# Kernel tuning notes

Measured on AMD Instinct MI355X. Metric: run time of the kernel, lower is better.

Reference implementation:

```python
import jax, jax.numpy as jnp
import numpy as np

IN_DIM = 512
OUT_DIM = 512


def setup_inputs() -> dict:
    key = jax.random.key(0)
    ks = jax.random.split(key, 7)
    B, S = 4, 2048
    scale = 1.0 / np.sqrt(IN_DIM)
    X = jax.random.normal(ks[0], (B, S, IN_DIM), dtype=jnp.float32)
    Wq = jax.random.normal(ks[1], (IN_DIM, OUT_DIM), dtype=jnp.float32) * scale
    Wk = jax.random.normal(ks[2], (IN_DIM, OUT_DIM), dtype=jnp.float32) * scale
    Wv = jax.random.normal(ks[3], (IN_DIM, OUT_DIM), dtype=jnp.float32) * scale
    bq = jnp.zeros((OUT_DIM,), dtype=jnp.float32)
    bk = jnp.zeros((OUT_DIM,), dtype=jnp.float32)
    bv = jnp.zeros((OUT_DIM,), dtype=jnp.float32)
    return {"X": X, "Wq": Wq, "bq": bq, "Wk": Wk, "bk": bk, "Wv": Wv, "bv": bv}


def reference(X, Wq, bq, Wk, bk, Wv, bv):
    # Q/K/V projections: [B,S,in] @ [in,out] -> [B,S,out]
    Q = X @ Wq + bq
    K = X @ Wk + bk
    V = X @ Wv + bv
    d_k = jnp.asarray(Q.shape[-1], Q.dtype)
    # scores: [B,S,S] = QK^T / sqrt(d_k)
    scores = jnp.einsum('bsd,btd->bst', Q, K) / jnp.sqrt(d_k)
    attn = jax.nn.softmax(scores, axis=-1)
    # out: [B,S,out]
    return jnp.einsum('bst,btd->bsd', attn, V)
```

## Files before the change

### kernel.cpp

```cpp
#include <hip/hip_runtime.h>
#include <hip/hip_bf16.h>
#include <stdint.h>

#define SEQ   2048
#define DIM   512
#define BATCH 4

typedef __attribute__((ext_vector_type(8))) short  short8;
typedef __attribute__((ext_vector_type(4))) float  floatx4;

static __device__ __forceinline__ unsigned short f2b(float f) {
  return __builtin_bit_cast(unsigned short, __float2bfloat16(f));
}

static __device__ __forceinline__ void gll16(const void* g, void* l) {
  __builtin_amdgcn_global_load_lds(
      (__attribute__((address_space(1))) void*)(uintptr_t)g,
      (__attribute__((address_space(3))) void*)l, 16, 0, 0);
}


template <int AF, int BF, int WM, int WN, int KC, int PH, int KIT, int NW>
__device__ __forceinline__ void fgemm_p(
    const char* __restrict__ A, int rtA0, int TKA,
    const char* __restrict__ B, int rtB0, int TKB,
    char* lds, floatx4 (&acc)[AF / WM][BF / WN])
{
  constexpr int AWF  = AF / WM, BWF = BF / WN;
  constexpr int SLOT = (AF + BF) * KC * 1024;
  constexpr int L    = KC * (AF / NW + BF / NW);
  constexpr int AC   = AWF / PH;
  static_assert(KIT >= 3, "pipeline needs >=3 K-slots");
  static_assert(AF % NW == 0 && BF % NW == 0, "frag rows must divide waves");
  static_assert(AWF % PH == 0 && L % PH == 0, "phase split must divide");
  const int tid = threadIdx.x;
  const int w = tid >> 6, l = tid & 63;
  const int wm = w % WM, wn = w / WM;

  auto stage_part = [&](char* dst, int kt, int p) {
#pragma unroll
    for (int g = p * (L / PH); g < (p + 1) * (L / PH); ++g) {
      if (g < KC * (AF / NW)) {
        const int c = g / (AF / NW), q = g % (AF / NW);
        const int f = q * NW + w;
        gll16(A + (((size_t)(rtA0 + f) * TKA + kt * KC + c) << 10) + l * 16,
              dst + (c * AF + f) * 1024 + l * 16);
      } else {
        const int h = g - KC * (AF / NW);
        const int c = h / (BF / NW), q = h % (BF / NW);
        const int f = q * NW + w;
        gll16(B + (((size_t)(rtB0 + f) * TKB + kt * KC + c) << 10) + l * 16,
              dst + (KC * AF + c * BF + f) * 1024 + l * 16);
      }
    }
  };

#pragma unroll
  for (int p = 0; p < PH; ++p) stage_part(lds, 0, p);
#pragma unroll
  for (int p = 0; p < PH; ++p) stage_part(lds + SLOT, 1, p);
  asm volatile("s_waitcnt vmcnt(%0) lgkmcnt(0)\ns_barrier" :: "n"(L) : "memory");

  short8 bf[KC][BWF];
  int cs = 0;
#pragma unroll 2
  for (int kt = 0; kt < KIT; ++kt) {
    const char* bA = lds + cs * SLOT;
    const char* bB = bA + KC * AF * 1024;
    int ns = cs - 1; if (ns < 0) ns = 2;
    char* pdst = lds + ns * SLOT;
#pragma unroll
    for (int p = 0; p < PH; ++p) {
      short8 af[KC][AC];
#pragma unroll
      for (int c = 0; c < KC; ++c)
#pragma unroll
        for (int i = 0; i < AC; ++i)
          af[c][i] = *(const short8*)(bA + (c * AF + wm * AWF + p * AC + i) * 1024 + l * 16);
      if (p == 0) {
#pragma unroll
        for (int c = 0; c < KC; ++c)
#pragma unroll
          for (int j = 0; j < BWF; ++j)
            bf[c][j] = *(const short8*)(bB + (c * BF + wn * BWF + j) * 1024 + l * 16);
      }
      if (kt + 2 < KIT) stage_part(pdst, kt + 2, p);

      asm volatile("s_barrier" ::: "memory");
      asm volatile("s_waitcnt lgkmcnt(0)" ::: "memory");
      __builtin_amdgcn_s_setprio(1);
#pragma unroll
      for (int c = 0; c < KC; ++c)
#pragma unroll
        for (int i = 0; i < AC; ++i)
#pragma unroll
          for (int j = 0; j < BWF; ++j)
            acc[p * AC + i][j] = __builtin_amdgcn_mfma_f32_16x16x32_bf16(
                af[c][i], bf[c][j], acc[p * AC + i][j], 0, 0, 0);
      __builtin_amdgcn_s_setprio(0);

      if (p == PH - 1) {
        if (kt + 2 < KIT)
          asm volatile("s_waitcnt vmcnt(%0)\ns_barrier" :: "n"(L) : "memory");
        else if (kt + 1 < KIT)
          asm volatile("s_waitcnt vmcnt(0)\ns_barrier" ::: "memory");
      } else {
        asm volatile("s_barrier" ::: "memory");
      }
    }
    ++cs; if (cs == 3) cs = 0;
  }
}

__global__ __launch_bounds__(256) void setup_kernel(
    const float* __restrict__ X, const float* __restrict__ Wq,
    const float* __restrict__ Wk, const float* __restrict__ Wv,
    short8* __restrict__ XbF, short8* __restrict__ WF)
{
  const int flat = blockIdx.x * 256 + threadIdx.x;
  {
    const int tile = flat >> 6, l = flat & 63;
    const int row = (tile >> 4) * 16 + (l & 15);
    const int k0  = (tile & 15) * 32 + (l >> 4) * 8;
    const float4 v0 = *(const float4*)(X + (size_t)row * DIM + k0);
    const float4 v1 = *(const float4*)(X + (size_t)row * DIM + k0 + 4);
    short8 o;
    o[0] = (short)f2b(v0.x); o[1] = (short)f2b(v0.y);
    o[2] = (short)f2b(v0.z); o[3] = (short)f2b(v0.w);
    o[4] = (short)f2b(v1.x); o[5] = (short)f2b(v1.y);
    o[6] = (short)f2b(v1.z); o[7] = (short)f2b(v1.w);
    XbF[flat] = o;
  }
  if (flat < 3 * 32768) {
    const int z = flat >> 15, within = flat & 32767;
    const float* W = (z == 0) ? Wq : (z == 1) ? Wk : Wv;
    const int tile = within >> 6, l = within & 63;
    const int n  = (tile >> 4) * 16 + (l & 15);
    const int k0 = (tile & 15) * 32 + (l >> 4) * 8;
    short8 o;
#pragma unroll
    for (int e = 0; e < 8; ++e)
      o[e] = (short)f2b(W[(size_t)(k0 + e) * DIM + n]);
    WF[flat] = o;
  }
}

__global__ __launch_bounds__(256, 2) void qkv_kernel(
    const short8* __restrict__ XbF, const short8* __restrict__ WF,
    const float* __restrict__ bq, const float* __restrict__ bk,
    const float* __restrict__ bv,
    unsigned short* __restrict__ QF, unsigned short* __restrict__ KF,
    unsigned short* __restrict__ VF)
{
  __shared__ char lds[73728];
  const int blk = blockIdx.x;
  const int n = (blk & 7) * 48 + (blk >> 3);
  const int lane = threadIdx.x & 63, w = threadIdx.x >> 6;
  const int wm = w & 1, wn = w >> 1;
  const char* Xc = (const char*)XbF;
  const char* Wc = (const char*)WF;
  floatx4 acc[8][4] = {};

  if (n < 256) {
    const int z = n >> 7, y = (n >> 6) & 1, x = n & 63;
    fgemm_p<16, 8, 2, 2, 1, 2, 16, 4>(Wc + (size_t)z * 524288, y * 16, 16,
                                      Xc, x * 8, 16, lds, acc);
    const float* bias = z ? bk : bq;
    unsigned short* OF = z ? KF : QF;
    const int dbase = y * 256 + wm * 128;
    const int sbase = x * 128 + wn * 64;
#pragma unroll
    for (int i2 = 0; i2 < 8; ++i2) {
      const int d0 = dbase + i2 * 16 + (lane >> 4) * 4;
      const float4 b4 = *(const float4*)(bias + d0);
#pragma unroll
      for (int j = 0; j < 4; ++j) {
        const int s = sbase + j * 16 + (lane & 15);
        ushort4 pk;
        pk.x = f2b(acc[i2][j][0] + b4.x);
        pk.y = f2b(acc[i2][j][1] + b4.y);
        pk.z = f2b(acc[i2][j][2] + b4.z);
        pk.w = f2b(acc[i2][j][3] + b4.w);
        *(ushort4*)(OF + (size_t)((s >> 4) * 16 + (d0 >> 5)) * 512 +
                    ((((d0 & 31) >> 3) << 4) | (s & 15)) * 8 + (d0 & 7)) = pk;
      }
    }
  } else {
    const int m = n - 256;
    const int x = m >> 2, y = m & 3;
    fgemm_p<16, 8, 2, 2, 1, 2, 16, 4>(Xc, x * 16, 16,
                                      Wc + 2 * 524288, y * 8, 16, lds, acc);
    const int sbase = x * 256 + wm * 128;
    const int dbase = y * 128 + wn * 64;
#pragma unroll
    for (int i2 = 0; i2 < 8; ++i2) {
      const int s0 = sbase + i2 * 16 + (lane >> 4) * 4;
      const int bt = s0 >> 11, t0 = s0 & 2047;
#pragma unroll
      for (int j = 0; j < 4; ++j) {
        const int d = dbase + j * 16 + (lane & 15);
        const float bn = bv[d];
        ushort4 pk;
        pk.x = f2b(acc[i2][j][0] + bn);
        pk.y = f2b(acc[i2][j][1] + bn);
        pk.z = f2b(acc[i2][j][2] + bn);
        pk.w = f2b(acc[i2][j][3] + bn);
        *(ushort4*)(VF + (size_t)bt * DIM * SEQ +
                    (size_t)((d >> 4) * 64 + (t0 >> 5)) * 512 +
                    ((((t0 & 31) >> 3) << 4) | (d & 15)) * 8 + (t0 & 7)) = pk;
      }
    }
  }
}

__global__ __launch_bounds__(512, 2) void scores_kernel(
    const unsigned short* __restrict__ QF, const unsigned short* __restrict__ KF,
    unsigned short* __restrict__ ScF, float* __restrict__ prow)
{
  __shared__ char lds[98304];
  const int blk = blockIdx.x;
  const int n = (blk & 7) * 32 + (blk >> 3);
  const int b = n >> 6, y = (n >> 3) & 7, x = n & 7;
  const int lane = threadIdx.x & 63, w = threadIdx.x >> 6;
  const int wm = w & 1, wn = w >> 1;
  floatx4 acc[8][4] = {};
  fgemm_p<16, 16, 2, 4, 1, 2, 16, 8>((const char*)KF + (size_t)b * 2097152, y * 16, 16,
                                     (const char*)QF + (size_t)b * 2097152, x * 16, 16,
                                     lds, acc);

  unsigned short* S = ScF + (size_t)b * SEQ * SEQ;
  const float scale = 0.044194173824159216f;
  const int tbase = y * 256 + wm * 128;
  const int sbase = x * 256 + wn * 64;
  float colsum[4] = {0.f, 0.f, 0.f, 0.f};
#pragma unroll
  for (int i2 = 0; i2 < 8; ++i2) {
    const int t0 = tbase + i2 * 16 + (lane >> 4) * 4;
#pragma unroll
    for (int j = 0; j < 4; ++j) {
      const int s = sbase + j * 16 + (lane & 15);
      float e0 = __expf(acc[i2][j][0] * scale);
      float e1 = __expf(acc[i2][j][1] * scale);
      float e2 = __expf(acc[i2][j][2] * scale);
      float e3 = __expf(acc[i2][j][3] * scale);
      colsum[j] += (e0 + e1) + (e2 + e3);
      ushort4 pk;
      pk.x = f2b(e0); pk.y = f2b(e1); pk.z = f2b(e2); pk.w = f2b(e3);
      *(ushort4*)(S + (size_t)((s >> 4) * 64 + (t0 >> 5)) * 512 +
                  ((((t0 & 31) >> 3) << 4) | (s & 15)) * 8 + (t0 & 7)) = pk;
    }
  }
#pragma unroll
  for (int j = 0; j < 4; ++j) {
    colsum[j] += __shfl_xor(colsum[j], 16, 64);
    colsum[j] += __shfl_xor(colsum[j], 32, 64);
  }
  if (lane < 16) {
    float* dst = prow + ((size_t)(y * 2 + wm) * BATCH + b) * SEQ + sbase + lane;
#pragma unroll
    for (int j = 0; j < 4; ++j) dst[j * 16] = colsum[j];
  }
}

__global__ __launch_bounds__(512, 2) void pv_kernel(
    const unsigned short* __restrict__ ScF, const unsigned short* __restrict__ VF,
    const float* __restrict__ prow, float* __restrict__ out)
{
  __shared__ char lds[98304];
  __shared__ float rinv[128];
  const int blk = blockIdx.x;
  const int n = (blk & 7) * 32 + (blk >> 3);
  const int b = n >> 6, x = (n >> 2) & 15, y = n & 3;
  const int t = threadIdx.x;
  if (t < 128) {
    const int s = x * 128 + t;
    float rr = 0.f;
#pragma unroll
    for (int q = 0; q < 16; ++q) rr += prow[((size_t)q * BATCH + b) * SEQ + s];
    rinv[t] = 1.f / rr;
  }
  const int lane = threadIdx.x & 63, w = threadIdx.x >> 6;
  const int wm = w & 1, wn = w >> 1;
  floatx4 acc[4][2] = {};
  fgemm_p<8, 8, 2, 4, 2, 1, 32, 8>((const char*)ScF + (size_t)b * 8388608, x * 8, 64,
                                   (const char*)VF + (size_t)b * 2097152, y * 8, 64,
                                   lds, acc);

  const int mbase = x * 128 + wm * 64;
  const int dbase = y * 128 + wn * 32;
#pragma unroll
  for (int i2 = 0; i2 < 4; ++i2) {
    const int r0 = wm * 64 + i2 * 16 + (lane >> 4) * 4;
    const int m0 = mbase + i2 * 16 + (lane >> 4) * 4;
    const float inv0 = rinv[r0], inv1 = rinv[r0 + 1], inv2 = rinv[r0 + 2], inv3 = rinv[r0 + 3];
#pragma unroll
    for (int j = 0; j < 2; ++j) {
      const int d = dbase + j * 16 + (lane & 15);
      float* o = out + ((size_t)b * SEQ + m0) * DIM + d;
      o[0 * DIM] = acc[i2][j][0] * inv0;
      o[1 * DIM] = acc[i2][j][1] * inv1;
      o[2 * DIM] = acc[i2][j][2] * inv2;
      o[3 * DIM] = acc[i2][j][3] * inv3;
    }
  }
}

extern "C" void kernel_launch(void* const* d_in, const int* in_sizes, int n_in,
                              void* d_out, int out_size, void* d_ws, size_t ws_size,
                              hipStream_t stream) {
  const float* X  = (const float*)d_in[0];
  const float* Wq = (const float*)d_in[1];
  const float* bq = (const float*)d_in[2];
  const float* Wk = (const float*)d_in[3];
  const float* bk = (const float*)d_in[4];
  const float* Wv = (const float*)d_in[5];
  const float* bv = (const float*)d_in[6];
  float* out = (float*)d_out;
  char* ws = (char*)d_ws;

  short8* XbF = (short8*)(ws + 0);
  float*  prow = (float*)(ws + 0);
  short8* WF  = (short8*)(ws + 8388608);
  unsigned short* QF  = (unsigned short*)(ws + 9961472);
  unsigned short* KF  = (unsigned short*)(ws + 18350080);
  unsigned short* VF  = (unsigned short*)(ws + 26738688);
  unsigned short* ScF = (unsigned short*)(ws + 35127296);

  setup_kernel<<<dim3(2048), 256, 0, stream>>>(X, Wq, Wk, Wv, XbF, WF);
  qkv_kernel<<<dim3(384), 256, 0, stream>>>(XbF, WF, bq, bk, bv, QF, KF, VF);
  scores_kernel<<<dim3(256), 512, 0, stream>>>(QF, KF, ScF, prow);
  pv_kernel<<<dim3(256), 512, 0, stream>>>(ScF, VF, prow, out);
}
```

Before: 140.7 us.

## Replace LDS-staged GEMM pipeline with direct global-to-register fragment loads

Drops the triple-buffered global_load_lds staging and its barriers. Each wave now loads its MFMA fragments straight from global memory into registers, using optional register double-buffering in the PV GEMM. The retiling gives qkv 8 waves per block and the scores kernel 512 blocks with narrower tiles, so the prow partial count goes from 16 to 32. Fragments shared across waves are no longer reused through LDS, which means more redundant global/L2 traffic and more exposed load latency in exchange for having no synchronisation.

After: 155.2 us. 10.4% more time.

```diff
diff --git a/kernel.cpp b/kernel.cpp
--- a/kernel.cpp
+++ b/kernel.cpp
@@ -13,102 +13,55 @@
   return __builtin_bit_cast(unsigned short, __float2bfloat16(f));
 }
 
-static __device__ __forceinline__ void gll16(const void* g, void* l) {
-  __builtin_amdgcn_global_load_lds(
-      (__attribute__((address_space(1))) void*)(uintptr_t)g,
-      (__attribute__((address_space(3))) void*)l, 16, 0, 0);
-}
-
-
-template <int AF, int BF, int WM, int WN, int KC, int PH, int KIT, int NW>
-__device__ __forceinline__ void fgemm_p(
+template <int AF, int BF, int WM, int WN, int KIT, bool DB>
+__device__ __forceinline__ void fgemm_d(
     const char* __restrict__ A, int rtA0, int TKA,
     const char* __restrict__ B, int rtB0, int TKB,
-    char* lds, floatx4 (&acc)[AF / WM][BF / WN])
-{
-  constexpr int AWF  = AF / WM, BWF = BF / WN;
-  constexpr int SLOT = (AF + BF) * KC * 1024;
-  constexpr int L    = KC * (AF / NW + BF / NW);
-  constexpr int AC   = AWF / PH;
-  static_assert(KIT >= 3, "pipeline needs >=3 K-slots");
-  static_assert(AF % NW == 0 && BF % NW == 0, "frag rows must divide waves");
-  static_assert(AWF % PH == 0 && L % PH == 0, "phase split must divide");
+    floatx4 (&acc)[AF / WM][BF / WN])
+{
+  constexpr int AWF = AF / WM, BWF = BF / WN;
   const int tid = threadIdx.x;
   const int w = tid >> 6, l = tid & 63;
   const int wm = w % WM, wn = w / WM;
-
-  auto stage_part = [&](char* dst, int kt, int p) {
-#pragma unroll
-    for (int g = p * (L / PH); g < (p + 1) * (L / PH); ++g) {
-      if (g < KC * (AF / NW)) {
-        const int c = g / (AF / NW), q = g % (AF / NW);
-        const int f = q * NW + w;
-        gll16(A + (((size_t)(rtA0 + f) * TKA + kt * KC + c) << 10) + l * 16,
-              dst + (c * AF + f) * 1024 + l * 16);
-      } else {
-        const int h = g - KC * (AF / NW);
-        const int c = h / (BF / NW), q = h % (BF / NW);
-        const int f = q * NW + w;
-        gll16(B + (((size_t)(rtB0 + f) * TKB + kt * KC + c) << 10) + l * 16,
-              dst + (KC * AF + c * BF + f) * 1024 + l * 16);
-      }
-    }
+  const char* Ab = A + (((size_t)(rtA0 + wm * AWF) * TKA) << 10) + l * 16;
+  const char* Bb = B + (((size_t)(rtB0 + wn * BWF) * TKB) << 10) + l * 16;
+
+  auto lda = [&](short8 (&af)[AWF], int kt) {
+#pragma unroll
+    for (int i = 0; i < AWF; ++i)
+      af[i] = *(const short8*)(Ab + (((size_t)i * TKA + kt) << 10));
   };
-
-#pragma unroll
-  for (int p = 0; p < PH; ++p) stage_part(lds, 0, p);
-#pragma unroll
-  for (int p = 0; p < PH; ++p) stage_part(lds + SLOT, 1, p);
-  asm volatile("s_waitcnt vmcnt(%0) lgkmcnt(0)\ns_barrier" :: "n"(L) : "memory");
-
-  short8 bf[KC][BWF];
-  int cs = 0;
+  auto ldb = [&](short8 (&bf)[BWF], int kt) {
+#pragma unroll
+    for (int j = 0; j < BWF; ++j)
+      bf[j] = *(const short8*)(Bb + (((size_t)j * TKB + kt) << 10));
+  };
+  auto domfma = [&](short8 (&af)[AWF], short8 (&bf)[BWF]) {
+#pragma unroll
+    for (int i = 0; i < AWF; ++i)
+#pragma unroll
+      for (int j = 0; j < BWF; ++j)
+        acc[i][j] = __builtin_amdgcn_mfma_f32_16x16x32_bf16(af[i], bf[j], acc[i][j], 0, 0, 0);
+  };
+
+  if constexpr (DB) {
+    short8 a0[AWF], b0[BWF], a1[AWF], b1[BWF];
+    lda(a0, 0); ldb(b0, 0);
+    static_assert(KIT % 2 == 0, "DB path needs even KIT");
 #pragma unroll 2
-  for (int kt = 0; kt < KIT; ++kt) {
-    const char* bA = lds + cs * SLOT;
-    const char* bB = bA + KC * AF * 1024;
-    int ns = cs - 1; if (ns < 0) ns = 2;
-    char* pdst = lds + ns * SLOT;
-#pragma unroll
-    for (int p = 0; p < PH; ++p) {
-      short8 af[KC][AC];
-#pragma unroll
-      for (int c = 0; c < KC; ++c)
-#pragma unroll
-        for (int i = 0; i < AC; ++i)
-          af[c][i] = *(const short8*)(bA + (c * AF + wm * AWF + p * AC + i) * 1024 + l * 16);
-      if (p == 0) {
-#pragma unroll
-        for (int c = 0; c < KC; ++c)
-#pragma unroll
-          for (int j = 0; j < BWF; ++j)
-            bf[c][j] = *(const short8*)(bB + (c * BF + wn * BWF + j) * 1024 + l * 16);
-      }
-      if (kt + 2 < KIT) stage_part(pdst, kt + 2, p);
-
-      asm volatile("s_barrier" ::: "memory");
-      asm volatile("s_waitcnt lgkmcnt(0)" ::: "memory");
-      __builtin_amdgcn_s_setprio(1);
-#pragma unroll
-      for (int c = 0; c < KC; ++c)
-#pragma unroll
-        for (int i = 0; i < AC; ++i)
-#pragma unroll
-          for (int j = 0; j < BWF; ++j)
-            acc[p * AC + i][j] = __builtin_amdgcn_mfma_f32_16x16x32_bf16(
-                af[c][i], bf[c][j], acc[p * AC + i][j], 0, 0, 0);
-      __builtin_amdgcn_s_setprio(0);
-
-      if (p == PH - 1) {
-        if (kt + 2 < KIT)
-          asm volatile("s_waitcnt vmcnt(%0)\ns_barrier" :: "n"(L) : "memory");
-        else if (kt + 1 < KIT)
-          asm volatile("s_waitcnt vmcnt(0)\ns_barrier" ::: "memory");
-      } else {
-        asm volatile("s_barrier" ::: "memory");
-      }
-    }
-    ++cs; if (cs == 3) cs = 0;
+    for (int kt = 0; kt < KIT; kt += 2) {
+      lda(a1, kt + 1); ldb(b1, kt + 1);
+      domfma(a0, b0);
+      if (kt + 2 < KIT) { lda(a0, kt + 2); ldb(b0, kt + 2); }
+      domfma(a1, b1);
+    }
+  } else {
+#pragma unroll 2
+    for (int kt = 0; kt < KIT; ++kt) {
+      short8 af[AWF], bf[BWF];
+      lda(af, kt); ldb(bf, kt);
+      domfma(af, bf);
+    }
   }
 }
 
@@ -145,32 +98,31 @@
   }
 }
 
-__global__ __launch_bounds__(256, 2) void qkv_kernel(
+__global__ __launch_bounds__(512, 2) void qkv_kernel(
     const short8* __restrict__ XbF, const short8* __restrict__ WF,
     const float* __restrict__ bq, const float* __restrict__ bk,
     const float* __restrict__ bv,
     unsigned short* __restrict__ QF, unsigned short* __restrict__ KF,
     unsigned short* __restrict__ VF)
 {
-  __shared__ char lds[73728];
   const int blk = blockIdx.x;
   const int n = (blk & 7) * 48 + (blk >> 3);
   const int lane = threadIdx.x & 63, w = threadIdx.x >> 6;
-  const int wm = w & 1, wn = w >> 1;
+  const int wm = w & 3, wn = w >> 2;
   const char* Xc = (const char*)XbF;
   const char* Wc = (const char*)WF;
-  floatx4 acc[8][4] = {};
+  floatx4 acc[4][4] = {};
 
   if (n < 256) {
     const int z = n >> 7, y = (n >> 6) & 1, x = n & 63;
-    fgemm_p<16, 8, 2, 2, 1, 2, 16, 4>(Wc + (size_t)z * 524288, y * 16, 16,
-                                      Xc, x * 8, 16, lds, acc);
+    fgemm_d<16, 8, 4, 2, 16, false>(Wc + (size_t)z * 524288, y * 16, 16,
+                                    Xc, x * 8, 16, acc);
     const float* bias = z ? bk : bq;
     unsigned short* OF = z ? KF : QF;
-    const int dbase = y * 256 + wm * 128;
+    const int dbase = y * 256 + wm * 64;
     const int sbase = x * 128 + wn * 64;
 #pragma unroll
-    for (int i2 = 0; i2 < 8; ++i2) {
+    for (int i2 = 0; i2 < 4; ++i2) {
       const int d0 = dbase + i2 * 16 + (lane >> 4) * 4;
       const float4 b4 = *(const float4*)(bias + d0);
 #pragma unroll
@@ -188,12 +140,12 @@
   } else {
     const int m = n - 256;
     const int x = m >> 2, y = m & 3;
-    fgemm_p<16, 8, 2, 2, 1, 2, 16, 4>(Xc, x * 16, 16,
-                                      Wc + 2 * 524288, y * 8, 16, lds, acc);
-    const int sbase = x * 256 + wm * 128;
+    fgemm_d<16, 8, 4, 2, 16, false>(Xc, x * 16, 16,
+                                    Wc + 2 * 524288, y * 8, 16, acc);
+    const int sbase = x * 256 + wm * 64;
     const int dbase = y * 128 + wn * 64;
 #pragma unroll
-    for (int i2 = 0; i2 < 8; ++i2) {
+    for (int i2 = 0; i2 < 4; ++i2) {
       const int s0 = sbase + i2 * 16 + (lane >> 4) * 4;
       const int bt = s0 >> 11, t0 = s0 & 2047;
 #pragma unroll
@@ -217,24 +169,24 @@
     const unsigned short* __restrict__ QF, const unsigned short* __restrict__ KF,
     unsigned short* __restrict__ ScF, float* __restrict__ prow)
 {
-  __shared__ char lds[98304];
   const int blk = blockIdx.x;
-  const int n = (blk & 7) * 32 + (blk >> 3);
-  const int b = n >> 6, y = (n >> 3) & 7, x = n & 7;
+  const int n = (blk & 7) * 64 + (blk >> 3);
+  const int b = n >> 7, t = n & 127;
+  const int y = t >> 4, x = t & 15;
   const int lane = threadIdx.x & 63, w = threadIdx.x >> 6;
-  const int wm = w & 1, wn = w >> 1;
-  floatx4 acc[8][4] = {};
-  fgemm_p<16, 16, 2, 4, 1, 2, 16, 8>((const char*)KF + (size_t)b * 2097152, y * 16, 16,
-                                     (const char*)QF + (size_t)b * 2097152, x * 16, 16,
-                                     lds, acc);
+  const int wm = w & 3, wn = w >> 2;
+  floatx4 acc[4][4] = {};
+  fgemm_d<16, 8, 4, 2, 16, false>((const char*)KF + (size_t)b * 2097152, y * 16, 16,
+                                  (const char*)QF + (size_t)b * 2097152, x * 8, 16,
+                                  acc);
 
   unsigned short* S = ScF + (size_t)b * SEQ * SEQ;
   const float scale = 0.044194173824159216f;
-  const int tbase = y * 256 + wm * 128;
-  const int sbase = x * 256 + wn * 64;
+  const int tbase = y * 256 + wm * 64;
+  const int sbase = x * 128 + wn * 64;
   float colsum[4] = {0.f, 0.f, 0.f, 0.f};
 #pragma unroll
-  for (int i2 = 0; i2 < 8; ++i2) {
+  for (int i2 = 0; i2 < 4; ++i2) {
     const int t0 = tbase + i2 * 16 + (lane >> 4) * 4;
 #pragma unroll
     for (int j = 0; j < 4; ++j) {
@@ -256,7 +208,7 @@
     colsum[j] += __shfl_xor(colsum[j], 32, 64);
   }
   if (lane < 16) {
-    float* dst = prow + ((size_t)(y * 2 + wm) * BATCH + b) * SEQ + sbase + lane;
+    float* dst = prow + ((size_t)(y * 4 + wm) * BATCH + b) * SEQ + sbase + lane;
 #pragma unroll
     for (int j = 0; j < 4; ++j) dst[j * 16] = colsum[j];
   }
@@ -266,35 +218,36 @@
     const unsigned short* __restrict__ ScF, const unsigned short* __restrict__ VF,
     const float* __restrict__ prow, float* __restrict__ out)
 {
-  __shared__ char lds[98304];
   __shared__ float rinv[128];
   const int blk = blockIdx.x;
   const int n = (blk & 7) * 32 + (blk >> 3);
-  const int b = n >> 6, x = (n >> 2) & 15, y = n & 3;
+  const int b = n >> 6, r = n & 63;
+  const int x = r >> 2, y = r & 3;
   const int t = threadIdx.x;
   if (t < 128) {
     const int s = x * 128 + t;
     float rr = 0.f;
 #pragma unroll
-    for (int q = 0; q < 16; ++q) rr += prow[((size_t)q * BATCH + b) * SEQ + s];
+    for (int q = 0; q < 32; ++q) rr += prow[((size_t)q * BATCH + b) * SEQ + s];
     rinv[t] = 1.f / rr;
   }
+  __syncthreads();
   const int lane = threadIdx.x & 63, w = threadIdx.x >> 6;
-  const int wm = w & 1, wn = w >> 1;
-  floatx4 acc[4][2] = {};
-  fgemm_p<8, 8, 2, 4, 2, 1, 32, 8>((const char*)ScF + (size_t)b * 8388608, x * 8, 64,
-                                   (const char*)VF + (size_t)b * 2097152, y * 8, 64,
-                                   lds, acc);
-
-  const int mbase = x * 128 + wm * 64;
-  const int dbase = y * 128 + wn * 32;
-#pragma unroll
-  for (int i2 = 0; i2 < 4; ++i2) {
-    const int r0 = wm * 64 + i2 * 16 + (lane >> 4) * 4;
+  const int wm = w & 3, wn = w >> 2;
+  floatx4 acc[2][4] = {};
+  fgemm_d<8, 8, 4, 2, 64, true>((const char*)ScF + (size_t)b * 8388608, x * 8, 64,
+                                (const char*)VF + (size_t)b * 2097152, y * 8, 64,
+                                acc);
+
+  const int mbase = x * 128 + wm * 32;
+  const int dbase = y * 128 + wn * 64;
+#pragma unroll
+  for (int i2 = 0; i2 < 2; ++i2) {
+    const int r0 = wm * 32 + i2 * 16 + (lane >> 4) * 4;
     const int m0 = mbase + i2 * 16 + (lane >> 4) * 4;
     const float inv0 = rinv[r0], inv1 = rinv[r0 + 1], inv2 = rinv[r0 + 2], inv3 = rinv[r0 + 3];
 #pragma unroll
-    for (int j = 0; j < 2; ++j) {
+    for (int j = 0; j < 4; ++j) {
       const int d = dbase + j * 16 + (lane & 15);
       float* o = out + ((size_t)b * SEQ + m0) * DIM + d;
       o[0 * DIM] = acc[i2][j][0] * inv0;
@@ -327,7 +280,7 @@
   unsigned short* ScF = (unsigned short*)(ws + 35127296);
 
   setup_kernel<<<dim3(2048), 256, 0, stream>>>(X, Wq, Wk, Wv, XbF, WF);
-  qkv_kernel<<<dim3(384), 256, 0, stream>>>(XbF, WF, bq, bk, bv, QF, KF, VF);
-  scores_kernel<<<dim3(256), 512, 0, stream>>>(QF, KF, ScF, prow);
+  qkv_kernel<<<dim3(384), 512, 0, stream>>>(XbF, WF, bq, bk, bv, QF, KF, VF);
+  scores_kernel<<<dim3(512), 512, 0, stream>>>(QF, KF, ScF, prow);
   pv_kernel<<<dim3(256), 512, 0, stream>>>(ScF, VF, prow, out);
 }
```
